# Optimization experiments

Hardware: AMD Instinct MI355X
Metric: run time of the kernel (lower is better)

## Reference

```python
import jax, jax.numpy as jnp
import numpy as np

D_MODEL = 1024
NUM_HEADS = 16
D_K = D_MODEL // NUM_HEADS


def setup_inputs() -> dict:
    key = jax.random.key(0)
    ks = jax.random.split(key, 11)
    B, S = 4, 2048
    s = 1.0 / np.sqrt(D_MODEL)
    return {
        "query": jax.random.normal(ks[0], (B, S, D_MODEL), jnp.float32),
        "key_in": jax.random.normal(ks[1], (B, S, D_MODEL), jnp.float32),
        "value": jax.random.normal(ks[2], (B, S, D_MODEL), jnp.float32),
        "Wq": jax.random.normal(ks[3], (D_MODEL, D_MODEL), jnp.float32) * s,
        "bq": jnp.zeros((D_MODEL,), jnp.float32),
        "Wk": jax.random.normal(ks[4], (D_MODEL, D_MODEL), jnp.float32) * s,
        "bk": jnp.zeros((D_MODEL,), jnp.float32),
        "Wv": jax.random.normal(ks[5], (D_MODEL, D_MODEL), jnp.float32) * s,
        "bv": jnp.zeros((D_MODEL,), jnp.float32),
        "Wo": jax.random.normal(ks[6], (D_MODEL, D_MODEL), jnp.float32) * s,
        "bo": jnp.zeros((D_MODEL,), jnp.float32),
    }


def _split_heads(x):
    # (B, S, d_model) -> (B, H, S, d_k)
    B, S, _ = x.shape
    return x.reshape(B, S, NUM_HEADS, D_K).transpose(0, 2, 1, 3)


def reference(query, key_in, value, Wq, bq, Wk, bk, Wv, bv, Wo, bo):
    # Linear projections (torch nn.Linear: x @ W.T + b)
    Q = _split_heads(query @ Wq.T + bq)   # (B, H, Sq, d_k)
    K = _split_heads(key_in @ Wk.T + bk)  # (B, H, Sk, d_k)
    V = _split_heads(value @ Wv.T + bv)   # (B, H, Sk, d_k)
    # Scaled dot-product attention (mask=None path)
    scores = jnp.einsum('bhqd,bhkd->bhqk', Q, K) / jnp.sqrt(jnp.float32(D_K))
    attn = jax.nn.softmax(scores, axis=-1)
    out = jnp.einsum('bhqk,bhkd->bhqd', attn, V)  # (B, H, Sq, d_k)
    B, H, Sq, _ = out.shape
    out = out.transpose(0, 2, 1, 3).reshape(B, Sq, D_MODEL)
    return out @ Wo.T + bo
```

## Files before the change

kernel.cpp:

```cpp
#include <hip/hip_runtime.h>


#define DMODEL 1024
#define DK     64
#define NH     16
#define BSZ    4
#define SEQ    2048
#define MTOT   (BSZ * SEQ)

typedef __attribute__((ext_vector_type(8))) __bf16 bf16x8;
typedef __attribute__((ext_vector_type(4))) float  f32x4;

__device__ inline unsigned short f2bf(float x) {
    union { float f; unsigned u; } v; v.f = x;
    unsigned r = v.u + 0x7FFF + ((v.u >> 16) & 1u);
    return (unsigned short)(r >> 16);
}

__device__ inline bf16x8 ld_frag(const unsigned short* p) {
    return __builtin_bit_cast(bf16x8, *(const int4*)p);
}

union V8 { int4 v; unsigned short s[8]; };
union V4 { uint2 v; unsigned short s[4]; };

__device__ inline void gload16(const unsigned short* g, unsigned short* l) {
    __builtin_amdgcn_global_load_lds(
        (const __attribute__((address_space(1))) void*)g,
        (__attribute__((address_space(3))) void*)l, 16, 0, 0);
}

__global__ __launch_bounds__(256)
void conv_bf16(const float* __restrict__ src, unsigned short* __restrict__ dst)
{
    int i = blockIdx.x * 256 + threadIdx.x;
    const float4* s = (const float4*)src + (size_t)i * 2;
    float4 a = s[0], b = s[1];
    V8 u;
    u.s[0] = f2bf(a.x); u.s[1] = f2bf(a.y); u.s[2] = f2bf(a.z); u.s[3] = f2bf(a.w);
    u.s[4] = f2bf(b.x); u.s[5] = f2bf(b.y); u.s[6] = f2bf(b.z); u.s[7] = f2bf(b.w);
    ((int4*)dst)[i] = u.v;
}

template<int OUT_F32, int BIAS_ROW>
__global__ __launch_bounds__(256)
void gemm_bt16(const unsigned short* __restrict__ A, const unsigned short* __restrict__ Bt,
               const float* __restrict__ bias, void* __restrict__ Cout,
               int Mdim, int Ndim, int Kdim)
{
    __shared__ unsigned short As[128 * 64];
    __shared__ unsigned short Bs[128 * 64];

    const int tid  = threadIdx.x;
    const int wave = tid >> 6, lane = tid & 63, quad = lane >> 4, l16 = lane & 15;
    const int wm = wave >> 1, wn = wave & 1;
    const int m0 = blockIdx.x * 128, n0 = blockIdx.y * 128;

    const int srow = lane >> 3;
    const int pch  = lane & 7;

    f32x4 acc[4][4];
#pragma unroll
    for (int i = 0; i < 4; ++i)
#pragma unroll
        for (int j = 0; j < 4; ++j)
#pragma unroll
            for (int r = 0; r < 4; ++r) acc[i][j][r] = 0.f;

    for (int k0 = 0; k0 < Kdim; k0 += 64) {
#pragma unroll
        for (int rr = 0; rr < 4; ++rr) {
            int row = rr * 32 + wave * 8 + srow;
            int c   = pch ^ (row & 7);
            unsigned short* lb = &As[(size_t)(rr * 32 + wave * 8) * 64];
            gload16(A + (size_t)(m0 + row) * Kdim + k0 + c * 8, lb);
        }
#pragma unroll
        for (int rr = 0; rr < 4; ++rr) {
            int row = rr * 32 + wave * 8 + srow;
            int c   = pch ^ (row & 7);
            unsigned short* lb = &Bs[(size_t)(rr * 32 + wave * 8) * 64];
            gload16(Bt + (size_t)(n0 + row) * Kdim + k0 + c * 8, lb);
        }
        __syncthreads();

#pragma unroll
        for (int hh = 0; hh < 2; ++hh) {
            bf16x8 af[4], bfr[4];
#pragma unroll
            for (int t = 0; t < 4; ++t) {
                int ra = wm * 64 + t * 16 + l16;
                int pa = (hh * 4 + quad) ^ (l16 & 7);
                af[t] = ld_frag(&As[(size_t)ra * 64 + pa * 8]);
                int rb = wn * 64 + t * 16 + l16;
                bfr[t] = ld_frag(&Bs[(size_t)rb * 64 + pa * 8]);
            }
#pragma unroll
            for (int i = 0; i < 4; ++i)
#pragma unroll
                for (int j = 0; j < 4; ++j)
                    acc[i][j] = __builtin_amdgcn_mfma_f32_16x16x32_bf16(af[i], bfr[j], acc[i][j], 0, 0, 0);
        }
        __syncthreads();
    }

#pragma unroll
    for (int j = 0; j < 4; ++j) {
        int n = n0 + wn * 64 + j * 16 + l16;
        float bcol = BIAS_ROW ? 0.f : bias[n];
#pragma unroll
        for (int i = 0; i < 4; ++i) {
#pragma unroll
            for (int r = 0; r < 4; ++r) {
                int m = m0 + wm * 64 + i * 16 + quad * 4 + r;
                float bv = BIAS_ROW ? bias[m] : bcol;
                float val = acc[i][j][r] + bv;
                if (OUT_F32) ((float*)Cout)[(size_t)m * Ndim + n] = val;
                else ((unsigned short*)Cout)[(size_t)m * Ndim + n] = f2bf(val);
            }
        }
    }
}

__global__ __launch_bounds__(256)
void attn_kernel(const unsigned short* __restrict__ Qb, const unsigned short* __restrict__ Kb,
                 const unsigned short* __restrict__ VbT, unsigned short* __restrict__ Ob)
{
    __shared__ unsigned short Ks[64][72];
    __shared__ unsigned short Vt[64][72];
    __shared__ unsigned short Ps[4][32][72];

    const int tid  = threadIdx.x;
    const int wave = tid >> 6, lane = tid & 63, quad = lane >> 4, l16 = lane & 15;
    const int q0 = blockIdx.x * 128, h = blockIdx.y, b = blockIdx.z;

    bf16x8 qf[2][2];
    const unsigned short* qbase = Qb + (size_t)(b * SEQ + q0 + wave * 32) * DMODEL + h * DK;
#pragma unroll
    for (int qs = 0; qs < 2; ++qs)
#pragma unroll
        for (int hh = 0; hh < 2; ++hh)
            qf[qs][hh] = ld_frag(qbase + (size_t)(qs * 16 + l16) * DMODEL + hh * 32 + quad * 8);

    f32x4 o[2][4], lacc[2];
#pragma unroll
    for (int qs = 0; qs < 2; ++qs) {
#pragma unroll
        for (int r = 0; r < 4; ++r) lacc[qs][r] = 0.f;
#pragma unroll
        for (int t = 0; t < 4; ++t)
#pragma unroll
            for (int r = 0; r < 4; ++r) o[qs][t][r] = 0.f;
    }

    bf16x8 onesf;
    {
        V8 u;
#pragma unroll
        for (int j = 0; j < 8; ++j) u.s[j] = 0x3F80;
        onesf = __builtin_bit_cast(bf16x8, u.v);
    }

    const int srow = tid >> 2;
    const int soff = (tid & 3) * 16;
    const int krow = 16 * (srow & 3) + (srow >> 2);

    for (int kt = 0; kt < SEQ; kt += 64) {
        __syncthreads();
        {
            const int4* kp = (const int4*)(Kb + (size_t)(b * SEQ + kt + srow) * DMODEL + h * DK + soff);
            const int4* vp = (const int4*)(VbT + (size_t)(h * DK + srow) * MTOT + b * SEQ + kt + soff);
            int4 k0 = kp[0], k1 = kp[1];
            int4 v0 = vp[0], v1 = vp[1];
            *(int4*)&Ks[krow][soff]     = k0;
            *(int4*)&Ks[krow][soff + 8] = k1;
            *(int4*)&Vt[srow][soff]     = v0;
            *(int4*)&Vt[srow][soff + 8] = v1;
        }
        __syncthreads();

        f32x4 s[2][4];
#pragma unroll
        for (int qs = 0; qs < 2; ++qs)
#pragma unroll
            for (int c = 0; c < 4; ++c)
#pragma unroll
                for (int r = 0; r < 4; ++r) s[qs][c][r] = 0.f;
#pragma unroll
        for (int c = 0; c < 4; ++c)
#pragma unroll
            for (int hh = 0; hh < 2; ++hh) {
                bf16x8 kb = ld_frag(&Ks[c * 16 + l16][hh * 32 + quad * 8]);
                s[0][c] = __builtin_amdgcn_mfma_f32_16x16x32_bf16(qf[0][hh], kb, s[0][c], 0, 0, 0);
                s[1][c] = __builtin_amdgcn_mfma_f32_16x16x32_bf16(qf[1][hh], kb, s[1][c], 0, 0, 0);
            }

#pragma unroll
        for (int qs = 0; qs < 2; ++qs)
#pragma unroll
            for (int r = 0; r < 4; ++r) {
                V4 pk;
#pragma unroll
                for (int c = 0; c < 4; ++c)
                    pk.s[c] = f2bf(exp2f(s[qs][c][r] * 0.18033688f));
                *(uint2*)&Ps[wave][qs * 16 + quad * 4 + r][4 * l16] = pk.v;
            }

        bf16x8 pf[2][2];
#pragma unroll
        for (int qs = 0; qs < 2; ++qs)
#pragma unroll
            for (int hh = 0; hh < 2; ++hh)
                pf[qs][hh] = ld_frag(&Ps[wave][qs * 16 + l16][hh * 32 + quad * 8]);

#pragma unroll
        for (int qs = 0; qs < 2; ++qs) {
            lacc[qs] = __builtin_amdgcn_mfma_f32_16x16x32_bf16(pf[qs][0], onesf, lacc[qs], 0, 0, 0);
            lacc[qs] = __builtin_amdgcn_mfma_f32_16x16x32_bf16(pf[qs][1], onesf, lacc[qs], 0, 0, 0);
        }

#pragma unroll
        for (int t = 0; t < 4; ++t)
#pragma unroll
            for (int hh = 0; hh < 2; ++hh) {
                bf16x8 vb = ld_frag(&Vt[t * 16 + l16][hh * 32 + quad * 8]);
                o[0][t] = __builtin_amdgcn_mfma_f32_16x16x32_bf16(pf[0][hh], vb, o[0][t], 0, 0, 0);
                o[1][t] = __builtin_amdgcn_mfma_f32_16x16x32_bf16(pf[1][hh], vb, o[1][t], 0, 0, 0);
            }
    }

#pragma unroll
    for (int qs = 0; qs < 2; ++qs) {
        float inv[4];
#pragma unroll
        for (int r = 0; r < 4; ++r) inv[r] = 1.f / lacc[qs][r];
#pragma unroll
        for (int t = 0; t < 4; ++t) {
            int d = h * DK + t * 16 + l16;
#pragma unroll
            for (int r = 0; r < 4; ++r) {
                int q = q0 + wave * 32 + qs * 16 + quad * 4 + r;
                Ob[(size_t)(b * SEQ + q) * DMODEL + d] = f2bf(o[qs][t][r] * inv[r]);
            }
        }
    }
}

extern "C" void kernel_launch(void* const* d_in, const int* in_sizes, int n_in,
                              void* d_out, int out_size, void* d_ws, size_t ws_size,
                              hipStream_t stream)
{
    const float* query  = (const float*)d_in[0];
    const float* key_in = (const float*)d_in[1];
    const float* value  = (const float*)d_in[2];
    const float* Wq = (const float*)d_in[3];
    const float* bq = (const float*)d_in[4];
    const float* Wk = (const float*)d_in[5];
    const float* bk = (const float*)d_in[6];
    const float* Wv = (const float*)d_in[7];
    const float* bv = (const float*)d_in[8];
    const float* Wo = (const float*)d_in[9];
    const float* bo = (const float*)d_in[10];

    const size_t NM = (size_t)MTOT * DMODEL;
    const size_t NW = (size_t)DMODEL * DMODEL;
    unsigned short* tmpA = (unsigned short*)d_ws;
    unsigned short* tmpW = tmpA + NM;
    unsigned short* Qb   = tmpW + NW;
    unsigned short* Kb   = Qb + NM;
    unsigned short* VbT  = Kb + NM;
    unsigned short* Ob   = tmpA;

    dim3 bb(256);
    const int gcA = (int)(NM / 8 / 256);
    const int gcW = (int)(NW / 8 / 256);
    dim3 gg(MTOT / 128, DMODEL / 128);
    dim3 gv(DMODEL / 128, MTOT / 128);

    conv_bf16<<<gcA, bb, 0, stream>>>(query, tmpA);
    conv_bf16<<<gcW, bb, 0, stream>>>(Wq, tmpW);
    gemm_bt16<0, 0><<<gg, bb, 0, stream>>>(tmpA, tmpW, bq, Qb, MTOT, DMODEL, DMODEL);

    conv_bf16<<<gcA, bb, 0, stream>>>(key_in, tmpA);
    conv_bf16<<<gcW, bb, 0, stream>>>(Wk, tmpW);
    gemm_bt16<0, 0><<<gg, bb, 0, stream>>>(tmpA, tmpW, bk, Kb, MTOT, DMODEL, DMODEL);

    conv_bf16<<<gcA, bb, 0, stream>>>(value, tmpA);
    conv_bf16<<<gcW, bb, 0, stream>>>(Wv, tmpW);
    gemm_bt16<0, 1><<<gv, bb, 0, stream>>>(tmpW, tmpA, bv, VbT, DMODEL, MTOT, DMODEL);

    attn_kernel<<<dim3(SEQ / 128, NH, BSZ), bb, 0, stream>>>(Qb, Kb, VbT, Ob);

    conv_bf16<<<gcW, bb, 0, stream>>>(Wo, tmpW);
    gemm_bt16<1, 0><<<gg, bb, 0, stream>>>(Ob, tmpW, bo, d_out, MTOT, DMODEL, DMODEL);
}
```

Before: 429.8 us.

## Fold softmax scale into Q projection, async swizzled K/V loads, cheaper exp/pack

The softmax scale (1/sqrt(dk)*log2e) moves into the Q projection GEMM epilogue, so the attention kernel calls the hardware exp2 directly on raw scores. K and V tiles are now loaded straight from global memory into LDS with global_load_lds, using an XOR-swizzled layout in place of padded arrays, which removes the register round trip. The float-to-bf16 packing of probabilities switches from round-to-nearest-even to a cheaper add-and-permute rounding. This lowers VALU and LDS staging work in the attention inner loop, at a small cost in rounding accuracy, and it changes where Q is rounded.

```diff
diff --git a/kernel.cpp b/kernel.cpp
--- a/kernel.cpp
+++ b/kernel.cpp
@@ -22,12 +22,17 @@
 }
 
 union V8 { int4 v; unsigned short s[8]; };
-union V4 { uint2 v; unsigned short s[4]; };
 
 __device__ inline void gload16(const unsigned short* g, unsigned short* l) {
     __builtin_amdgcn_global_load_lds(
         (const __attribute__((address_space(1))) void*)g,
         (__attribute__((address_space(3))) void*)l, 16, 0, 0);
+}
+
+__device__ inline unsigned pack_bf(float lo, float hi) {
+    unsigned b0 = __builtin_bit_cast(unsigned, lo) + 0x8000u;
+    unsigned b1 = __builtin_bit_cast(unsigned, hi) + 0x8000u;
+    return __builtin_amdgcn_perm(b1, b0, 0x07060302u);
 }
 
 __global__ __launch_bounds__(256)
@@ -46,7 +51,7 @@
 __global__ __launch_bounds__(256)
 void gemm_bt16(const unsigned short* __restrict__ A, const unsigned short* __restrict__ Bt,
                const float* __restrict__ bias, void* __restrict__ Cout,
-               int Mdim, int Ndim, int Kdim)
+               int Mdim, int Ndim, int Kdim, float scale)
 {
     __shared__ unsigned short As[128 * 64];
     __shared__ unsigned short Bs[128 * 64];
@@ -72,15 +77,15 @@
         for (int rr = 0; rr < 4; ++rr) {
             int row = rr * 32 + wave * 8 + srow;
             int c   = pch ^ (row & 7);
-            unsigned short* lb = &As[(size_t)(rr * 32 + wave * 8) * 64];
-            gload16(A + (size_t)(m0 + row) * Kdim + k0 + c * 8, lb);
+            gload16(A + (size_t)(m0 + row) * Kdim + k0 + c * 8,
+                    &As[(size_t)(rr * 32 + wave * 8) * 64]);
         }
 #pragma unroll
         for (int rr = 0; rr < 4; ++rr) {
             int row = rr * 32 + wave * 8 + srow;
             int c   = pch ^ (row & 7);
-            unsigned short* lb = &Bs[(size_t)(rr * 32 + wave * 8) * 64];
-            gload16(Bt + (size_t)(n0 + row) * Kdim + k0 + c * 8, lb);
+            gload16(Bt + (size_t)(n0 + row) * Kdim + k0 + c * 8,
+                    &Bs[(size_t)(rr * 32 + wave * 8) * 64]);
         }
         __syncthreads();
 
@@ -114,7 +119,7 @@
             for (int r = 0; r < 4; ++r) {
                 int m = m0 + wm * 64 + i * 16 + quad * 4 + r;
                 float bv = BIAS_ROW ? bias[m] : bcol;
-                float val = acc[i][j][r] + bv;
+                float val = (acc[i][j][r] + bv) * scale;
                 if (OUT_F32) ((float*)Cout)[(size_t)m * Ndim + n] = val;
                 else ((unsigned short*)Cout)[(size_t)m * Ndim + n] = f2bf(val);
             }
@@ -126,13 +131,14 @@
 void attn_kernel(const unsigned short* __restrict__ Qb, const unsigned short* __restrict__ Kb,
                  const unsigned short* __restrict__ VbT, unsigned short* __restrict__ Ob)
 {
-    __shared__ unsigned short Ks[64][72];
-    __shared__ unsigned short Vt[64][72];
+    __shared__ unsigned short Ks[64 * 64];
+    __shared__ unsigned short Vt[64 * 64];
     __shared__ unsigned short Ps[4][32][72];
 
     const int tid  = threadIdx.x;
     const int wave = tid >> 6, lane = tid & 63, quad = lane >> 4, l16 = lane & 15;
     const int q0 = blockIdx.x * 128, h = blockIdx.y, b = blockIdx.z;
+    const int sw = l16 & 7;
 
     bf16x8 qf[2][2];
     const unsigned short* qbase = Qb + (size_t)(b * SEQ + q0 + wave * 32) * DMODEL + h * DK;
@@ -142,15 +148,16 @@
         for (int hh = 0; hh < 2; ++hh)
             qf[qs][hh] = ld_frag(qbase + (size_t)(qs * 16 + l16) * DMODEL + hh * 32 + quad * 8);
 
+    f32x4 zero4;
+#pragma unroll
+    for (int r = 0; r < 4; ++r) zero4[r] = 0.f;
+
     f32x4 o[2][4], lacc[2];
 #pragma unroll
     for (int qs = 0; qs < 2; ++qs) {
-#pragma unroll
-        for (int r = 0; r < 4; ++r) lacc[qs][r] = 0.f;
-#pragma unroll
-        for (int t = 0; t < 4; ++t)
-#pragma unroll
-            for (int r = 0; r < 4; ++r) o[qs][t][r] = 0.f;
+        lacc[qs] = zero4;
+#pragma unroll
+        for (int t = 0; t < 4; ++t) o[qs][t] = zero4;
     }
 
     bf16x8 onesf;
@@ -161,49 +168,47 @@
         onesf = __builtin_bit_cast(bf16x8, u.v);
     }
 
-    const int srow = tid >> 2;
-    const int soff = (tid & 3) * 16;
-    const int krow = 16 * (srow & 3) + (srow >> 2);
+    const int sr  = lane >> 3;
+    const int pch = lane & 7;
 
     for (int kt = 0; kt < SEQ; kt += 64) {
         __syncthreads();
-        {
-            const int4* kp = (const int4*)(Kb + (size_t)(b * SEQ + kt + srow) * DMODEL + h * DK + soff);
-            const int4* vp = (const int4*)(VbT + (size_t)(h * DK + srow) * MTOT + b * SEQ + kt + soff);
-            int4 k0 = kp[0], k1 = kp[1];
-            int4 v0 = vp[0], v1 = vp[1];
-            *(int4*)&Ks[krow][soff]     = k0;
-            *(int4*)&Ks[krow][soff + 8] = k1;
-            *(int4*)&Vt[srow][soff]     = v0;
-            *(int4*)&Vt[srow][soff + 8] = v1;
+#pragma unroll
+        for (int i = 0; i < 2; ++i) {
+            int blk = wave * 2 + i;
+            int row = blk * 8 + sr;
+            int c   = pch ^ (row & 7);
+            int key = 4 * (row & 15) + (row >> 4);
+            gload16(Kb + (size_t)(b * SEQ + kt + key) * DMODEL + h * DK + c * 8,
+                    &Ks[(size_t)blk * 512]);
+            gload16(VbT + (size_t)(h * DK + row) * MTOT + b * SEQ + kt + c * 8,
+                    &Vt[(size_t)blk * 512]);
         }
         __syncthreads();
 
         f32x4 s[2][4];
 #pragma unroll
+        for (int c = 0; c < 4; ++c) {
+            bf16x8 kb0 = ld_frag(&Ks[(size_t)(c * 16 + l16) * 64 + ((quad ^ sw) * 8)]);
+            bf16x8 kb1 = ld_frag(&Ks[(size_t)(c * 16 + l16) * 64 + (((4 + quad) ^ sw) * 8)]);
+            s[0][c] = __builtin_amdgcn_mfma_f32_16x16x32_bf16(qf[0][1], kb1,
+                      __builtin_amdgcn_mfma_f32_16x16x32_bf16(qf[0][0], kb0, zero4, 0, 0, 0), 0, 0, 0);
+            s[1][c] = __builtin_amdgcn_mfma_f32_16x16x32_bf16(qf[1][1], kb1,
+                      __builtin_amdgcn_mfma_f32_16x16x32_bf16(qf[1][0], kb0, zero4, 0, 0, 0), 0, 0, 0);
+        }
+
+#pragma unroll
         for (int qs = 0; qs < 2; ++qs)
 #pragma unroll
-            for (int c = 0; c < 4; ++c)
-#pragma unroll
-                for (int r = 0; r < 4; ++r) s[qs][c][r] = 0.f;
-#pragma unroll
-        for (int c = 0; c < 4; ++c)
-#pragma unroll
-            for (int hh = 0; hh < 2; ++hh) {
-                bf16x8 kb = ld_frag(&Ks[c * 16 + l16][hh * 32 + quad * 8]);
-                s[0][c] = __builtin_amdgcn_mfma_f32_16x16x32_bf16(qf[0][hh], kb, s[0][c], 0, 0, 0);
-                s[1][c] = __builtin_amdgcn_mfma_f32_16x16x32_bf16(qf[1][hh], kb, s[1][c], 0, 0, 0);
-            }
-
-#pragma unroll
-        for (int qs = 0; qs < 2; ++qs)
-#pragma unroll
             for (int r = 0; r < 4; ++r) {
-                V4 pk;
-#pragma unroll
-                for (int c = 0; c < 4; ++c)
-                    pk.s[c] = f2bf(exp2f(s[qs][c][r] * 0.18033688f));
-                *(uint2*)&Ps[wave][qs * 16 + quad * 4 + r][4 * l16] = pk.v;
+                float p0 = __builtin_amdgcn_exp2f(s[qs][0][r]);
+                float p1 = __builtin_amdgcn_exp2f(s[qs][1][r]);
+                float p2 = __builtin_amdgcn_exp2f(s[qs][2][r]);
+                float p3 = __builtin_amdgcn_exp2f(s[qs][3][r]);
+                uint2 pk;
+                pk.x = pack_bf(p0, p1);
+                pk.y = pack_bf(p2, p3);
+                *(uint2*)&Ps[wave][qs * 16 + quad * 4 + r][4 * l16] = pk;
             }
 
         bf16x8 pf[2][2];
@@ -223,7 +228,7 @@
         for (int t = 0; t < 4; ++t)
 #pragma unroll
             for (int hh = 0; hh < 2; ++hh) {
-                bf16x8 vb = ld_frag(&Vt[t * 16 + l16][hh * 32 + quad * 8]);
+                bf16x8 vb = ld_frag(&Vt[(size_t)(t * 16 + l16) * 64 + (((hh * 4 + quad) ^ sw) * 8)]);
                 o[0][t] = __builtin_amdgcn_mfma_f32_16x16x32_bf16(pf[0][hh], vb, o[0][t], 0, 0, 0);
                 o[1][t] = __builtin_amdgcn_mfma_f32_16x16x32_bf16(pf[1][hh], vb, o[1][t], 0, 0, 0);
             }
@@ -277,20 +282,22 @@
     dim3 gg(MTOT / 128, DMODEL / 128);
     dim3 gv(DMODEL / 128, MTOT / 128);
 
+    const float qscale = 0.18033688f;
+
     conv_bf16<<<gcA, bb, 0, stream>>>(query, tmpA);
     conv_bf16<<<gcW, bb, 0, stream>>>(Wq, tmpW);
-    gemm_bt16<0, 0><<<gg, bb, 0, stream>>>(tmpA, tmpW, bq, Qb, MTOT, DMODEL, DMODEL);
+    gemm_bt16<0, 0><<<gg, bb, 0, stream>>>(tmpA, tmpW, bq, Qb, MTOT, DMODEL, DMODEL, qscale);
 
     conv_bf16<<<gcA, bb, 0, stream>>>(key_in, tmpA);
     conv_bf16<<<gcW, bb, 0, stream>>>(Wk, tmpW);
-    gemm_bt16<0, 0><<<gg, bb, 0, stream>>>(tmpA, tmpW, bk, Kb, MTOT, DMODEL, DMODEL);
+    gemm_bt16<0, 0><<<gg, bb, 0, stream>>>(tmpA, tmpW, bk, Kb, MTOT, DMODEL, DMODEL, 1.0f);
 
     conv_bf16<<<gcA, bb, 0, stream>>>(value, tmpA);
     conv_bf16<<<gcW, bb, 0, stream>>>(Wv, tmpW);
-    gemm_bt16<0, 1><<<gv, bb, 0, stream>>>(tmpW, tmpA, bv, VbT, DMODEL, MTOT, DMODEL);
+    gemm_bt16<0, 1><<<gv, bb, 0, stream>>>(tmpW, tmpA, bv, VbT, DMODEL, MTOT, DMODEL, 1.0f);
 
     attn_kernel<<<dim3(SEQ / 128, NH, BSZ), bb, 0, stream>>>(Qb, Kb, VbT, Ob);
 
     conv_bf16<<<gcW, bb, 0, stream>>>(Wo, tmpW);
-    gemm_bt16<1, 0><<<gg, bb, 0, stream>>>(Ob, tmpW, bo, d_out, MTOT, DMODEL, DMODEL);
-}
+    gemm_bt16<1, 0><<<gg, bb, 0, stream>>>(Ob, tmpW, bo, d_out, MTOT, DMODEL, DMODEL, 1.0f);
+}
```

Result: faster. 368.3 us (-14.3%).
